# Performance work log

Measured on AMD Instinct MI355X. Metric: run time of the kernel, lower is better.

The kernel has to match this reference:

```python
import jax, jax.numpy as jnp
import numpy as np

L = 4096
E = 512   # embed dim
S = 1024  # state dim
H = 150   # Scorer hidden dim
GI = 2 * S + E
MAX_N = 10


def _scorer(x, W1, b1, W2, b2, W3, b3):
    h = jax.nn.relu(x @ W1 + b1)
    h = jax.nn.relu(h @ W2 + b2)
    return h @ W3 + b3  # [..., 1]


def setup_inputs() -> dict:
    key = jax.random.key(0)
    ks = jax.random.split(key, 16)
    def init(k, shape, fan_in):
        return jax.random.normal(k, shape, dtype=jnp.float32) / np.sqrt(fan_in)
    inp = {
        "embeds": jax.random.normal(ks[0], (L, E), dtype=jnp.float32),
        "states": jax.random.normal(ks[1], (L, S), dtype=jnp.float32),
        # attention Scorer params (input S)
        "aW1": init(ks[2], (S, H), S), "ab1": jnp.zeros((H,), jnp.float32),
        "aW2": init(ks[3], (H, H), H), "ab2": jnp.zeros((H,), jnp.float32),
        "aW3": init(ks[4], (H, 1), H), "ab3": jnp.zeros((1,), jnp.float32),
        # sm Scorer params (input GI)
        "sW1": init(ks[5], (GI, H), GI), "sb1": jnp.zeros((H,), jnp.float32),
        "sW2": init(ks[6], (H, H), H), "sb2": jnp.zeros((H,), jnp.float32),
        "sW3": init(ks[7], (H, 1), H), "sb3": jnp.zeros((1,), jnp.float32),
    }
    return inp


def reference(embeds, states, aW1, ab1, aW2, ab2, aW3, ab3,
              sW1, sb1, sW2, sb2, sW3, sb3):
    # per-token attention logits, computed once: [L]
    attns = _scorer(states, aW1, ab1, aW2, ab2, aW3, ab3)[:, 0]

    gs = []
    for n in range(1, MAX_N + 1):  # fixed small loop over window sizes
        M = L - n + 1                                  # number of windows
        starts = jnp.arange(M)
        idx = starts[:, None] + jnp.arange(n)          # [M, n] token indices
        w = jax.nn.softmax(attns[idx], axis=1)         # windowed softmax [M, n]
        pooled = jnp.einsum('mn,mne->me', w, embeds[idx])  # [M, E]
        g = jnp.concatenate([states[starts], states[starts + n - 1], pooled],
                            axis=1)                    # [M, 2S+E]
        gs.append(g)
    x = jnp.concatenate(gs, axis=0)                    # [T, GI], T = 10L-45
    scores = _scorer(x, sW1, sb1, sW2, sb2, sW3, sb3)[:, 0]  # [T]
    return scores
```

## Files before the change

### kernel.cpp

```cpp
#include <hip/hip_runtime.h>
#include <math.h>

#define LTOK 4096
#define EDIM 512
#define SDIM 1024
#define HDIM 150
#define SEG 160
#define MAXN 10
#define TOTAL_ROWS 40915
#define KA 1536
#define NKT 48
#define K2 160
#define NCG 42

typedef _Float16 hfrag __attribute__((ext_vector_type(8)));
typedef float ffrag __attribute__((ext_vector_type(4)));


#define ITEMS_A   (LTOK * (KA / 8))
#define ITEMS_W   (NCG * NKT * 64)
#define ITEMS_W2  (K2 * (K2 / 8))
#define ITEMS_A2  (K2 * (K2 / 8))
#define ITEMS_TOT (ITEMS_A + ITEMS_W + ITEMS_W2 + ITEMS_A2)

__global__ __launch_bounds__(256) void prep_kernel(
    const float* __restrict__ embeds, const float* __restrict__ states,
    const float* __restrict__ aW1, const float* __restrict__ aW2,
    const float* __restrict__ sW1, const float* __restrict__ sW2,
    _Float16* __restrict__ Apk, _Float16* __restrict__ Wpk,
    _Float16* __restrict__ W2pk, _Float16* __restrict__ A2pk)
{
    int it = blockIdx.x * 256 + threadIdx.x;
    if (it < ITEMS_A) {
        const int rem = it % (NKT * 64);
        const int g = it / (NKT * 64), kt = rem >> 6, lane = rem & 63;
        const int row = g * 16 + (lane & 15);
        const int k0 = kt * 32 + (lane >> 4) * 8;
        const float* src = (k0 < SDIM) ? (states + (size_t)row * SDIM + k0)
                                       : (embeds + (size_t)row * EDIM + (k0 - SDIM));
        const float4 v0 = *(const float4*)src;
        const float4 v1 = *(const float4*)(src + 4);
        _Float16 o[8] = {(_Float16)v0.x, (_Float16)v0.y, (_Float16)v0.z, (_Float16)v0.w,
                         (_Float16)v1.x, (_Float16)v1.y, (_Float16)v1.z, (_Float16)v1.w};
        *(uint4*)(Apk + (size_t)it * 8) = *(uint4*)o;
        return;
    }
    it -= ITEMS_A;
    if (it < ITEMS_W) {
        const int rem = it % (NKT * 64);
        const int cgi = it / (NKT * 64), kt = rem >> 6, lane = rem & 63;
        const int col = cgi * 16 + (lane & 15);
        const int k0 = kt * 32 + (lane >> 4) * 8;
        _Float16 o[8];
        for (int j = 0; j < 8; ++j) {
            const int k = k0 + j;
            float wv = 0.f;
            if (col < 160) {
                if (col < HDIM && k < SDIM) wv = sW1[(size_t)k * HDIM + col];
            } else if (col < 320) {
                const int cj = col - 160;
                if (cj < HDIM && k < SDIM) wv = sW1[(size_t)(SDIM + k) * HDIM + cj];
            } else if (col < 480) {
                const int cj = col - 320;
                if (cj < HDIM && k >= SDIM) wv = sW1[(size_t)(SDIM + k) * HDIM + cj];
            } else if (col >= 512) {
                const int cj = col - 512;
                if (cj < HDIM && k < SDIM) wv = aW1[(size_t)k * HDIM + cj];
            }
            o[j] = (_Float16)wv;
        }
        *(uint4*)(Wpk + ((size_t)((size_t)cgi * NKT + kt) * 64 + lane) * 8) = *(uint4*)o;
        return;
    }
    it -= ITEMS_W;
    if (it < ITEMS_W2 + ITEMS_A2) {
        const bool is_a = (it >= ITEMS_W2);
        const int li = is_a ? (it - ITEMS_W2) : it;
        const float* src = is_a ? aW2 : sW2;
        _Float16* dst = is_a ? A2pk : W2pk;
        const int tk = li >> 6, lane = li & 63;
        const int col = (tk / 5) * 16 + (lane & 15);
        const int k0 = (tk % 5) * 32 + (lane >> 4) * 8;
        _Float16 o[8];
        for (int j = 0; j < 8; ++j) {
            const int k = k0 + j;
            float wv = (col < HDIM && k < HDIM) ? src[(size_t)k * HDIM + col] : 0.f;
            o[j] = (_Float16)wv;
        }
        *(uint4*)(dst + ((size_t)tk * 64 + lane) * 8) = *(uint4*)o;
    }
}

__global__ __launch_bounds__(256) void k_proj(
    const _Float16* __restrict__ Apk, const _Float16* __restrict__ Wpk,
    const _Float16* __restrict__ A2pk,
    const float* __restrict__ ab1, const float* __restrict__ ab2,
    const float* __restrict__ aW3, const float* __restrict__ ab3,
    _Float16* __restrict__ P1h, _Float16* __restrict__ P2h,
    _Float16* __restrict__ PEh, float* __restrict__ attns)
{
    const int bid = blockIdx.x;
    const int tid = threadIdx.x;
    const int w = tid >> 6, lane = tid & 63;
    const int quad = lane >> 4, l16 = lane & 15;

    __shared__ __align__(16) _Float16 ah1[64 * SEG];

    if (bid % 9 == 0) {
        const int tok0 = (bid / 9) * 64;
        const int g = tok0 / 16 + w;

        ffrag acc[10];
#pragma unroll
        for (int c = 0; c < 10; ++c) acc[c] = (ffrag){0.f, 0.f, 0.f, 0.f};

        const _Float16* ap = Apk + ((size_t)g * NKT) * 512 + lane * 8;
#pragma unroll 2
        for (int kt = 0; kt < 32; ++kt) {
            const hfrag a = *(const hfrag*)(ap + (size_t)kt * 512);
#pragma unroll
            for (int c = 0; c < 10; ++c) {
                const hfrag b = *(const hfrag*)(
                    Wpk + (((size_t)(32 + c) * NKT + kt) * 64 + lane) * 8);
                acc[c] = __builtin_amdgcn_mfma_f32_16x16x32_f16(a, b, acc[c], 0, 0, 0);
            }
        }
#pragma unroll
        for (int c = 0; c < 10; ++c) {
            const int col = c * 16 + l16;
            const float b1 = (col < HDIM) ? ab1[col] : 0.f;
#pragma unroll
            for (int r = 0; r < 4; ++r) {
                const int row = w * 16 + quad * 4 + r;
                ah1[row * SEG + col] = (_Float16)fmaxf(acc[c][r] + b1, 0.f);
            }
        }
        __syncthreads();

        hfrag af[5];
#pragma unroll
        for (int ks = 0; ks < 5; ++ks)
            af[ks] = *(const hfrag*)&ah1[(w * 16 + l16) * SEG + ks * 32 + quad * 8];

        float part[4] = {0.f, 0.f, 0.f, 0.f};
        for (int ct = 0; ct < 10; ++ct) {
            ffrag a2 = (ffrag){0.f, 0.f, 0.f, 0.f};
#pragma unroll
            for (int ks = 0; ks < 5; ++ks) {
                const hfrag fb = *(const hfrag*)(
                    A2pk + ((size_t)(ct * 5 + ks) * 64 + lane) * 8);
                a2 = __builtin_amdgcn_mfma_f32_16x16x32_f16(af[ks], fb, a2, 0, 0, 0);
            }
            const int col = ct * 16 + l16;
            const float s2 = (col < HDIM) ? ab2[col] : 0.f;
            const float s3 = (col < HDIM) ? aW3[col] : 0.f;
#pragma unroll
            for (int r = 0; r < 4; ++r) part[r] += fmaxf(a2[r] + s2, 0.f) * s3;
        }
#pragma unroll
        for (int off = 1; off < 16; off <<= 1) {
#pragma unroll
            for (int r = 0; r < 4; ++r) part[r] += __shfl_xor(part[r], off, 64);
        }
        if (l16 == 0) {
            const float b3 = ab3[0];
#pragma unroll
            for (int r = 0; r < 4; ++r)
                attns[tok0 + w * 16 + quad * 4 + r] = part[r] + b3;
        }
        return;
    }

    const int tile = bid - bid / 9 - 1;
    const int bM = tile & 63, bN = tile >> 6;
    const int wm = w & 1, wn = w >> 1;
    const int gbase = bM * 4 + wm * 2;
    const int cgbase = bN * 4 + wn * 2;
    if (cgbase >= 30) return;
    const int kt0 = (bN >= 5) ? 32 : 0;
    const int kt1 = (bN >= 5) ? 48 : 32;

    ffrag acc[2][2];
#pragma unroll
    for (int t = 0; t < 2; ++t)
#pragma unroll
        for (int u = 0; u < 2; ++u) acc[t][u] = (ffrag){0.f, 0.f, 0.f, 0.f};

    const _Float16* a0p = Apk + ((size_t)(gbase + 0) * NKT) * 512 + lane * 8;
    const _Float16* a1p = Apk + ((size_t)(gbase + 1) * NKT) * 512 + lane * 8;
    const _Float16* b0p = Wpk + ((size_t)(cgbase + 0) * NKT) * 512 + lane * 8;
    const _Float16* b1p = Wpk + ((size_t)(cgbase + 1) * NKT) * 512 + lane * 8;

#pragma unroll 8
    for (int kt = kt0; kt < kt1; ++kt) {
        const hfrag a0 = *(const hfrag*)(a0p + (size_t)kt * 512);
        const hfrag a1 = *(const hfrag*)(a1p + (size_t)kt * 512);
        const hfrag b0 = *(const hfrag*)(b0p + (size_t)kt * 512);
        const hfrag b1 = *(const hfrag*)(b1p + (size_t)kt * 512);
        acc[0][0] = __builtin_amdgcn_mfma_f32_16x16x32_f16(a0, b0, acc[0][0], 0, 0, 0);
        acc[1][0] = __builtin_amdgcn_mfma_f32_16x16x32_f16(a1, b0, acc[1][0], 0, 0, 0);
        acc[0][1] = __builtin_amdgcn_mfma_f32_16x16x32_f16(a0, b1, acc[0][1], 0, 0, 0);
        acc[1][1] = __builtin_amdgcn_mfma_f32_16x16x32_f16(a1, b1, acc[1][1], 0, 0, 0);
    }

#pragma unroll
    for (int t = 0; t < 2; ++t)
#pragma unroll
        for (int u = 0; u < 2; ++u) {
            const int col = (cgbase + u) * 16 + l16;
#pragma unroll
            for (int r = 0; r < 4; ++r) {
                const int row = (gbase + t) * 16 + quad * 4 + r;
                const _Float16 hv = (_Float16)acc[t][u][r];
                if (col < 160)      P1h[(size_t)row * SEG + col] = hv;
                else if (col < 320) P2h[(size_t)row * SEG + (col - 160)] = hv;
                else if (col < 480) PEh[(size_t)row * SEG + (col - 320)] = hv;
            }
        }
}

__global__ __launch_bounds__(256) void span_kernel(
    const float* __restrict__ attns, const _Float16* __restrict__ P1h,
    const _Float16* __restrict__ P2h, const _Float16* __restrict__ PEh,
    const float* __restrict__ sb1, const _Float16* __restrict__ W2pk,
    const float* __restrict__ sb2, const float* __restrict__ sW3,
    const float* __restrict__ sb3, float* __restrict__ out)
{
    const int pairI = blockIdx.x % 5;
    const int mChunk = blockIdx.x / 5;
    const int n0 = 2 * pairI + 1, n1 = n0 + 1;
    const int Mn0 = LTOK - n0 + 1, Mn1 = Mn0 - 1;
    const int m0 = mChunk * 32;
    const int offn0 = (n0 - 1) * LTOK - ((n0 - 1) * (n0 - 2)) / 2;
    const int offn1 = offn0 + Mn0;

    const int tid = threadIdx.x;
    const int w = tid >> 6, lane = tid & 63, quad = lane >> 4, l16 = lane & 15;

    __shared__ __align__(16) _Float16 h1h[2][32 * K2];
    __shared__ float wgt[2][32][MAXN];

    if (tid < 64) {
        const int q = tid >> 5, r = tid & 31;
        const int n = q ? n1 : n0;
        const int Mn = q ? Mn1 : Mn0;
        const int m = m0 + r;
        if (m < Mn) {
            float mx = -1e30f;
            for (int j = 0; j < n; ++j) mx = fmaxf(mx, attns[m + j]);
            float tp[MAXN]; float s = 0.f;
            for (int j = 0; j < n; ++j) { tp[j] = expf(attns[m + j] - mx); s += tp[j]; }
            const float inv = 1.f / s;
            for (int j = 0; j < MAXN; ++j) wgt[q][r][j] = (j < n) ? tp[j] * inv : 0.f;
        } else {
            for (int j = 0; j < MAXN; ++j) wgt[q][r][j] = 0.f;
        }
    }
    __syncthreads();

    for (int item = tid; item < 32 * (K2 / 8); item += 256) {
        const int r = item / (K2 / 8), cc = item % (K2 / 8);
        const int c0 = cc * 8;
        const int mm = m0 + r;
        const hfrag p1  = *(const hfrag*)(P1h + (size_t)mm * SEG + c0);
        const hfrag p2a = *(const hfrag*)(P2h + (size_t)min(mm + n0 - 1, LTOK - 1) * SEG + c0);
        const hfrag p2b = *(const hfrag*)(P2h + (size_t)min(mm + n0, LTOK - 1) * SEG + c0);
        float b1v[8];
#pragma unroll
        for (int e = 0; e < 8; ++e)
            b1v[e] = (c0 + e < HDIM) ? sb1[c0 + e] : 0.f;
        float a0[8], a1[8];
#pragma unroll
        for (int e = 0; e < 8; ++e) {
            a0[e] = (float)p1[e] + (float)p2a[e] + b1v[e];
            a1[e] = (float)p1[e] + (float)p2b[e] + b1v[e];
        }
#pragma unroll
        for (int j = 0; j < MAXN; ++j) {
            const int mj = min(mm + j, LTOK - 1);
            const hfrag pe = *(const hfrag*)(PEh + (size_t)mj * SEG + c0);
            const float w0j = wgt[0][r][j];
            const float w1j = wgt[1][r][j];
#pragma unroll
            for (int e = 0; e < 8; ++e) {
                const float pv = (float)pe[e];
                a0[e] = fmaf(w0j, pv, a0[e]);
                a1[e] = fmaf(w1j, pv, a1[e]);
            }
        }
        _Float16 o0[8], o1[8];
#pragma unroll
        for (int e = 0; e < 8; ++e) {
            const bool live = (c0 + e < HDIM);
            o0[e] = live ? (_Float16)fmaxf(a0[e], 0.f) : (_Float16)0.f;
            o1[e] = live ? (_Float16)fmaxf(a1[e], 0.f) : (_Float16)0.f;
        }
        *(uint4*)&h1h[0][r * K2 + c0] = *(uint4*)o0;
        *(uint4*)&h1h[1][r * K2 + c0] = *(uint4*)o1;
    }
    __syncthreads();

    const int q = w >> 1, rg = w & 1;
    const int Mq = q ? Mn1 : Mn0;
    const int offq = q ? offn1 : offn0;

    hfrag af[5];
#pragma unroll
    for (int ks = 0; ks < 5; ++ks)
        af[ks] = *(const hfrag*)&h1h[q][(rg * 16 + l16) * K2 + ks * 32 + quad * 8];

    float part[4] = {0.f, 0.f, 0.f, 0.f};
    for (int ct = 0; ct < 10; ++ct) {
        ffrag acc = (ffrag){0.f, 0.f, 0.f, 0.f};
#pragma unroll
        for (int ks = 0; ks < 5; ++ks) {
            const hfrag fb = *(const hfrag*)(
                W2pk + ((size_t)(ct * 5 + ks) * 64 + lane) * 8);
            acc = __builtin_amdgcn_mfma_f32_16x16x32_f16(af[ks], fb, acc, 0, 0, 0);
        }
        const int col = ct * 16 + l16;
        const float s2 = (col < HDIM) ? sb2[col] : 0.f;
        const float s3 = (col < HDIM) ? sW3[col] : 0.f;
#pragma unroll
        for (int r = 0; r < 4; ++r) part[r] += fmaxf(acc[r] + s2, 0.f) * s3;
    }

#pragma unroll
    for (int off = 1; off < 16; off <<= 1) {
#pragma unroll
        for (int r = 0; r < 4; ++r) part[r] += __shfl_xor(part[r], off, 64);
    }
    if (l16 == 0) {
        const float b3 = sb3[0];
#pragma unroll
        for (int r = 0; r < 4; ++r) {
            const int lr = rg * 16 + quad * 4 + r;
            if (m0 + lr < Mq) out[offq + m0 + lr] = part[r] + b3;
        }
    }
}

extern "C" void kernel_launch(void* const* d_in, const int* in_sizes, int n_in,
                              void* d_out, int out_size, void* d_ws, size_t ws_size,
                              hipStream_t stream) {
    const float* embeds = (const float*)d_in[0];
    const float* states = (const float*)d_in[1];
    const float* aW1 = (const float*)d_in[2];
    const float* ab1 = (const float*)d_in[3];
    const float* aW2 = (const float*)d_in[4];
    const float* ab2 = (const float*)d_in[5];
    const float* aW3 = (const float*)d_in[6];
    const float* ab3 = (const float*)d_in[7];
    const float* sW1 = (const float*)d_in[8];
    const float* sb1 = (const float*)d_in[9];
    const float* sW2 = (const float*)d_in[10];
    const float* sb2 = (const float*)d_in[11];
    const float* sW3 = (const float*)d_in[12];
    const float* sb3 = (const float*)d_in[13];
    float* out = (float*)d_out;

    float* attns = (float*)d_ws;
    _Float16* P1h  = (_Float16*)(attns + LTOK);
    _Float16* P2h  = P1h + (size_t)LTOK * SEG;
    _Float16* PEh  = P2h + (size_t)LTOK * SEG;
    _Float16* Apk  = PEh + (size_t)LTOK * SEG;
    _Float16* Wpk  = Apk + (size_t)ITEMS_A * 8;
    _Float16* W2pk = Wpk + (size_t)ITEMS_W * 8;
    _Float16* A2pk = W2pk + (size_t)ITEMS_W2 * 8;

    prep_kernel<<<ITEMS_TOT / 256, 256, 0, stream>>>(
        embeds, states, aW1, aW2, sW1, sW2, Apk, Wpk, W2pk, A2pk);
    k_proj<<<576, 256, 0, stream>>>(
        Apk, Wpk, A2pk, ab1, ab2, aW3, ab3, P1h, P2h, PEh, attns);
    span_kernel<<<640, 256, 0, stream>>>(
        attns, P1h, P2h, PEh, sb1, W2pk, sb2, sW3, sb3, out);
}
```

Before: 146.0 us.

## Stage projection GEMM tiles through double-buffered LDS with register prefetch

The projection GEMM tiles in k_proj now load their A and W fragments cooperatively into a double-buffered shared-memory tile. The next k-step is prefetched into registers, so each block reads each fragment from global memory once and waves share them, instead of every wave loading directly. Dead waves stay alive for the barriers and only skip the store. The softmax weight setup in span_kernel also preloads the attention logits into registers with unrolled, clamped loads. In exchange, the GEMM loop now has a block-wide barrier on every k-step, which may stall the MFMA pipeline.

```diff
diff --git a/kernel.cpp b/kernel.cpp
--- a/kernel.cpp
+++ b/kernel.cpp
@@ -104,9 +104,10 @@
     const int w = tid >> 6, lane = tid & 63;
     const int quad = lane >> 4, l16 = lane & 15;
 
-    __shared__ __align__(16) _Float16 ah1[64 * SEG];
+    __shared__ __align__(16) _Float16 smem[64 * SEG];
 
     if (bid % 9 == 0) {
+        _Float16* ah1 = smem;
         const int tok0 = (bid / 9) * 64;
         const int g = tok0 / 16 + w;
 
@@ -174,49 +175,89 @@
     const int tile = bid - bid / 9 - 1;
     const int bM = tile & 63, bN = tile >> 6;
     const int wm = w & 1, wn = w >> 1;
-    const int gbase = bM * 4 + wm * 2;
-    const int cgbase = bN * 4 + wn * 2;
-    if (cgbase >= 30) return;
+    const int gbase0 = bM * 4;
+    const int cgbase0 = bN * 4;
+    const int cgbase = cgbase0 + wn * 2;
+    const bool alive = (cgbase < 30);
     const int kt0 = (bN >= 5) ? 32 : 0;
     const int kt1 = (bN >= 5) ? 48 : 32;
 
+    _Float16* As = smem;
+    _Float16* Bs = smem + 4096;
+
+    const int sgrp = tid >> 6, sln = tid & 63;
+    const _Float16* aSrc = Apk + (((size_t)(gbase0 + sgrp) * NKT) * 64 + sln) * 8;
+    const _Float16* bSrc = Wpk + (((size_t)(cgbase0 + sgrp) * NKT) * 64 + sln) * 8;
+    const int sOff = (sgrp * 64 + sln) * 8;
+
     ffrag acc[2][2];
 #pragma unroll
     for (int t = 0; t < 2; ++t)
 #pragma unroll
         for (int u = 0; u < 2; ++u) acc[t][u] = (ffrag){0.f, 0.f, 0.f, 0.f};
 
-    const _Float16* a0p = Apk + ((size_t)(gbase + 0) * NKT) * 512 + lane * 8;
-    const _Float16* a1p = Apk + ((size_t)(gbase + 1) * NKT) * 512 + lane * 8;
-    const _Float16* b0p = Wpk + ((size_t)(cgbase + 0) * NKT) * 512 + lane * 8;
-    const _Float16* b1p = Wpk + ((size_t)(cgbase + 1) * NKT) * 512 + lane * 8;
-
-#pragma unroll 8
+    const int aOff0 = ((wm * 2 + 0) * 64 + lane) * 8;
+    const int aOff1 = ((wm * 2 + 1) * 64 + lane) * 8;
+    const int bOff0 = ((wn * 2 + 0) * 64 + lane) * 8;
+    const int bOff1 = ((wn * 2 + 1) * 64 + lane) * 8;
+
+    {
+        const uint4 va = *(const uint4*)(aSrc + (size_t)kt0 * 512);
+        const uint4 vb = *(const uint4*)(bSrc + (size_t)kt0 * 512);
+        *(uint4*)(As + sOff) = va;
+        *(uint4*)(Bs + sOff) = vb;
+    }
+    uint4 qa, qb;
+    if (kt0 + 1 < kt1) {
+        qa = *(const uint4*)(aSrc + (size_t)(kt0 + 1) * 512);
+        qb = *(const uint4*)(bSrc + (size_t)(kt0 + 1) * 512);
+    }
+    __syncthreads();
+
+    int buf = 0;
     for (int kt = kt0; kt < kt1; ++kt) {
-        const hfrag a0 = *(const hfrag*)(a0p + (size_t)kt * 512);
-        const hfrag a1 = *(const hfrag*)(a1p + (size_t)kt * 512);
-        const hfrag b0 = *(const hfrag*)(b0p + (size_t)kt * 512);
-        const hfrag b1 = *(const hfrag*)(b1p + (size_t)kt * 512);
+        uint4 na, nb;
+        const bool have2 = (kt + 2 < kt1);
+        const bool have1 = (kt + 1 < kt1);
+        if (have2) {
+            na = *(const uint4*)(aSrc + (size_t)(kt + 2) * 512);
+            nb = *(const uint4*)(bSrc + (size_t)(kt + 2) * 512);
+        }
+        if (have1) {
+            *(uint4*)(As + (buf ^ 1) * 2048 + sOff) = qa;
+            *(uint4*)(Bs + (buf ^ 1) * 2048 + sOff) = qb;
+        }
+        const _Float16* Ab = As + buf * 2048;
+        const _Float16* Bb = Bs + buf * 2048;
+        const hfrag a0 = *(const hfrag*)(Ab + aOff0);
+        const hfrag a1 = *(const hfrag*)(Ab + aOff1);
+        const hfrag b0 = *(const hfrag*)(Bb + bOff0);
+        const hfrag b1 = *(const hfrag*)(Bb + bOff1);
         acc[0][0] = __builtin_amdgcn_mfma_f32_16x16x32_f16(a0, b0, acc[0][0], 0, 0, 0);
         acc[1][0] = __builtin_amdgcn_mfma_f32_16x16x32_f16(a1, b0, acc[1][0], 0, 0, 0);
         acc[0][1] = __builtin_amdgcn_mfma_f32_16x16x32_f16(a0, b1, acc[0][1], 0, 0, 0);
         acc[1][1] = __builtin_amdgcn_mfma_f32_16x16x32_f16(a1, b1, acc[1][1], 0, 0, 0);
-    }
-
-#pragma unroll
-    for (int t = 0; t < 2; ++t)
-#pragma unroll
-        for (int u = 0; u < 2; ++u) {
-            const int col = (cgbase + u) * 16 + l16;
-#pragma unroll
-            for (int r = 0; r < 4; ++r) {
-                const int row = (gbase + t) * 16 + quad * 4 + r;
-                const _Float16 hv = (_Float16)acc[t][u][r];
-                if (col < 160)      P1h[(size_t)row * SEG + col] = hv;
-                else if (col < 320) P2h[(size_t)row * SEG + (col - 160)] = hv;
-                else if (col < 480) PEh[(size_t)row * SEG + (col - 320)] = hv;
-            }
-        }
+        __syncthreads();
+        qa = na; qb = nb;
+        buf ^= 1;
+    }
+
+    if (alive) {
+#pragma unroll
+        for (int t = 0; t < 2; ++t)
+#pragma unroll
+            for (int u = 0; u < 2; ++u) {
+                const int col = (cgbase + u) * 16 + l16;
+#pragma unroll
+                for (int r = 0; r < 4; ++r) {
+                    const int row = (gbase0 + wm * 2 + t) * 16 + quad * 4 + r;
+                    const _Float16 hv = (_Float16)acc[t][u][r];
+                    if (col < 160)      P1h[(size_t)row * SEG + col] = hv;
+                    else if (col < 320) P2h[(size_t)row * SEG + (col - 160)] = hv;
+                    else if (col < 480) PEh[(size_t)row * SEG + (col - 320)] = hv;
+                }
+            }
+    }
 }
 
 __global__ __launch_bounds__(256) void span_kernel(
@@ -246,10 +287,14 @@
         const int Mn = q ? Mn1 : Mn0;
         const int m = m0 + r;
         if (m < Mn) {
+            float av[MAXN];
+#pragma unroll
+            for (int j = 0; j < MAXN; ++j)
+                av[j] = attns[min(m + j, LTOK - 1)];
             float mx = -1e30f;
-            for (int j = 0; j < n; ++j) mx = fmaxf(mx, attns[m + j]);
+            for (int j = 0; j < n; ++j) mx = fmaxf(mx, av[j]);
             float tp[MAXN]; float s = 0.f;
-            for (int j = 0; j < n; ++j) { tp[j] = expf(attns[m + j] - mx); s += tp[j]; }
+            for (int j = 0; j < n; ++j) { tp[j] = expf(av[j] - mx); s += tp[j]; }
             const float inv = 1.f / s;
             for (int j = 0; j < MAXN; ++j) wgt[q][r][j] = (j < n) ? tp[j] * inv : 0.f;
         } else {
```

Measured after the change: 145.9 us. About the same (-0.1%).

## Software-pipeline MFMA loads in GEMM kernels and stage PE rows in LDS

Applied to the files above, without the earlier changes.

The attention-scorer and projection GEMM loops become double-buffered: the next k-tile's A/B fragments are loaded while MFMAs run on the current ones, aiming to hide global-load latency. The span kernel now copies the 41 PE rows its window range touches into shared memory once, instead of re-reading each row from global memory for all 10 offsets. It also preloads attention logits into registers for the softmax. The cost is more register pressure from the doubled fragment buffers and extra LDS use, which could lower occupancy.

```diff
diff --git a/kernel.cpp b/kernel.cpp
--- a/kernel.cpp
+++ b/kernel.cpp
@@ -15,6 +15,8 @@
 
 typedef _Float16 hfrag __attribute__((ext_vector_type(8)));
 typedef float ffrag __attribute__((ext_vector_type(4)));
+
+#define MFMA_(a, b, c) __builtin_amdgcn_mfma_f32_16x16x32_f16(a, b, c, 0, 0, 0)
 
 
 #define ITEMS_A   (LTOK * (KA / 8))
@@ -115,16 +117,34 @@
         for (int c = 0; c < 10; ++c) acc[c] = (ffrag){0.f, 0.f, 0.f, 0.f};
 
         const _Float16* ap = Apk + ((size_t)g * NKT) * 512 + lane * 8;
-#pragma unroll 2
+        const _Float16* wb = Wpk + lane * 8;
+
+#define LDA_(kt) (*(const hfrag*)(ap + (size_t)(kt) * 512))
+#define LOADC(BX, kt, h)                                                    \
+        _Pragma("unroll")                                                   \
+        for (int c_ = 0; c_ < 5; ++c_)                                      \
+            BX[c_] = *(const hfrag*)(wb +                                   \
+                ((size_t)(32 + (h) * 5 + c_) * NKT + (kt)) * 512);
+#define MFMA5(av, BX, h)                                                    \
+        _Pragma("unroll")                                                   \
+        for (int c_ = 0; c_ < 5; ++c_)                                      \
+            acc[(h) * 5 + c_] = MFMA_(av, BX[c_], acc[(h) * 5 + c_]);
+
+        hfrag aA = LDA_(0), aB;
+        hfrag bX[5], bY[5];
+        LOADC(bX, 0, 0);
         for (int kt = 0; kt < 32; ++kt) {
-            const hfrag a = *(const hfrag*)(ap + (size_t)kt * 512);
-#pragma unroll
-            for (int c = 0; c < 10; ++c) {
-                const hfrag b = *(const hfrag*)(
-                    Wpk + (((size_t)(32 + c) * NKT + kt) * 64 + lane) * 8);
-                acc[c] = __builtin_amdgcn_mfma_f32_16x16x32_f16(a, b, acc[c], 0, 0, 0);
-            }
-        }
+            LOADC(bY, kt, 1);
+            if (kt + 1 < 32) aB = LDA_(kt + 1);
+            MFMA5(aA, bX, 0);
+            if (kt + 1 < 32) LOADC(bX, kt + 1, 0);
+            MFMA5(aA, bY, 1);
+            aA = aB;
+        }
+#undef LDA_
+#undef LOADC
+#undef MFMA5
+
 #pragma unroll
         for (int c = 0; c < 10; ++c) {
             const int col = c * 16 + l16;
@@ -191,17 +211,35 @@
     const _Float16* b0p = Wpk + ((size_t)(cgbase + 0) * NKT) * 512 + lane * 8;
     const _Float16* b1p = Wpk + ((size_t)(cgbase + 1) * NKT) * 512 + lane * 8;
 
-#pragma unroll 8
-    for (int kt = kt0; kt < kt1; ++kt) {
-        const hfrag a0 = *(const hfrag*)(a0p + (size_t)kt * 512);
-        const hfrag a1 = *(const hfrag*)(a1p + (size_t)kt * 512);
-        const hfrag b0 = *(const hfrag*)(b0p + (size_t)kt * 512);
-        const hfrag b1 = *(const hfrag*)(b1p + (size_t)kt * 512);
-        acc[0][0] = __builtin_amdgcn_mfma_f32_16x16x32_f16(a0, b0, acc[0][0], 0, 0, 0);
-        acc[1][0] = __builtin_amdgcn_mfma_f32_16x16x32_f16(a1, b0, acc[1][0], 0, 0, 0);
-        acc[0][1] = __builtin_amdgcn_mfma_f32_16x16x32_f16(a0, b1, acc[0][1], 0, 0, 0);
-        acc[1][1] = __builtin_amdgcn_mfma_f32_16x16x32_f16(a1, b1, acc[1][1], 0, 0, 0);
-    }
+    hfrag Ax0[2], Ax1[2], Bx0[2], Bx1[2];
+    hfrag Ay0[2], Ay1[2], By0[2], By1[2];
+
+#define LOADB(A0_, A1_, B0_, B1_, kb)                                       \
+    _Pragma("unroll")                                                       \
+    for (int u_ = 0; u_ < 2; ++u_) {                                        \
+        A0_[u_] = *(const hfrag*)(a0p + (size_t)((kb) + u_) * 512);         \
+        A1_[u_] = *(const hfrag*)(a1p + (size_t)((kb) + u_) * 512);         \
+        B0_[u_] = *(const hfrag*)(b0p + (size_t)((kb) + u_) * 512);         \
+        B1_[u_] = *(const hfrag*)(b1p + (size_t)((kb) + u_) * 512);         \
+    }
+#define MFMAB(A0_, A1_, B0_, B1_)                                           \
+    _Pragma("unroll")                                                       \
+    for (int u_ = 0; u_ < 2; ++u_) {                                        \
+        acc[0][0] = MFMA_(A0_[u_], B0_[u_], acc[0][0]);                     \
+        acc[1][0] = MFMA_(A1_[u_], B0_[u_], acc[1][0]);                     \
+        acc[0][1] = MFMA_(A0_[u_], B1_[u_], acc[0][1]);                     \
+        acc[1][1] = MFMA_(A1_[u_], B1_[u_], acc[1][1]);                     \
+    }
+
+    LOADB(Ax0, Ax1, Bx0, Bx1, kt0);
+    for (int kb = kt0; kb < kt1; kb += 4) {
+        LOADB(Ay0, Ay1, By0, By1, kb + 2);
+        MFMAB(Ax0, Ax1, Bx0, Bx1);
+        if (kb + 4 < kt1) LOADB(Ax0, Ax1, Bx0, Bx1, kb + 4);
+        MFMAB(Ay0, Ay1, By0, By1);
+    }
+#undef LOADB
+#undef MFMAB
 
 #pragma unroll
     for (int t = 0; t < 2; ++t)
@@ -238,7 +276,15 @@
     const int w = tid >> 6, lane = tid & 63, quad = lane >> 4, l16 = lane & 15;
 
     __shared__ __align__(16) _Float16 h1h[2][32 * K2];
+    __shared__ __align__(16) _Float16 PEs[41 * SEG];
     __shared__ float wgt[2][32][MAXN];
+
+    for (int t = tid; t < 41 * (SEG / 8); t += 256) {
+        const int rr = t / (SEG / 8), cc = t % (SEG / 8);
+        const int srcRow = min(m0 + rr, LTOK - 1);
+        *(uint4*)&PEs[rr * SEG + cc * 8] =
+            *(const uint4*)(PEh + (size_t)srcRow * SEG + cc * 8);
+    }
 
     if (tid < 64) {
         const int q = tid >> 5, r = tid & 31;
@@ -246,10 +292,14 @@
         const int Mn = q ? Mn1 : Mn0;
         const int m = m0 + r;
         if (m < Mn) {
+            float av[MAXN];
+#pragma unroll
+            for (int j = 0; j < MAXN; ++j)
+                av[j] = attns[min(m + j, LTOK - 1)];
             float mx = -1e30f;
-            for (int j = 0; j < n; ++j) mx = fmaxf(mx, attns[m + j]);
+            for (int j = 0; j < n; ++j) mx = fmaxf(mx, av[j]);
             float tp[MAXN]; float s = 0.f;
-            for (int j = 0; j < n; ++j) { tp[j] = expf(attns[m + j] - mx); s += tp[j]; }
+            for (int j = 0; j < n; ++j) { tp[j] = expf(av[j] - mx); s += tp[j]; }
             const float inv = 1.f / s;
             for (int j = 0; j < MAXN; ++j) wgt[q][r][j] = (j < n) ? tp[j] * inv : 0.f;
         } else {
@@ -277,8 +327,7 @@
         }
 #pragma unroll
         for (int j = 0; j < MAXN; ++j) {
-            const int mj = min(mm + j, LTOK - 1);
-            const hfrag pe = *(const hfrag*)(PEh + (size_t)mj * SEG + c0);
+            const hfrag pe = *(const hfrag*)&PEs[(r + j) * SEG + c0];
             const float w0j = wgt[0][r][j];
             const float w1j = wgt[1][r][j];
 #pragma unroll
```

After: 144.6 us. About the same (-1.0%).
